# Kernel tuning notes

Measured on AMD Instinct MI355X. Metric: run time of the kernel, lower is better.

The kernel has to match this reference:

```python
import jax, jax.numpy as jnp
import numpy as np

PAA_SIZE = 64  # init_kwargs paa_size
GAF_TYPE = 'GADF'  # init_kwargs GAF_type


def setup_inputs() -> dict:
    key = jax.random.key(0)
    x = jax.random.uniform(key, (256, 4096, 32), dtype=jnp.float32)
    return {"x": x}


def reference(x):
    # x: [B, T, C]
    B, T, C = x.shape
    # --- rescale: per-sample, per-channel min-max over time axis -> [0, 1]
    x_min = jnp.min(x, axis=1, keepdims=True)
    x_max = jnp.max(x, axis=1, keepdims=True)
    r = (x - x_min) / (x_max - x_min)            # [B, T, C]
    # --- PAA: strided mean over bins of length size = T // paa_size
    size = T // PAA_SIZE
    p = r[:, : PAA_SIZE * size].reshape(B, PAA_SIZE, size, C).sum(axis=2) / size  # [B, P, C]
    # --- GAF construction
    y = jnp.sqrt(1.0 - p * p)                    # [B, P, C]
    if GAF_TYPE == 'GASF':
        # out[b,i,j,c] = x_i x_j - y_i y_j (symmetric)
        out = jnp.einsum('bic,bjc->bijc', p, p) - jnp.einsum('bic,bjc->bijc', y, y)
    else:  # 'GADF'
        # original: -transpose(y x^T - x y^T) => out[b,i,j,c] = y_i x_j - x_i y_j
        out = jnp.einsum('bic,bjc->bijc', y, p) - jnp.einsum('bic,bjc->bijc', p, y)
    return out  # [B, paa_size, paa_size, C]
```

## Files before the change

kernel.cpp:

```cpp
#include <hip/hip_runtime.h>
#include <math.h>

#define BB   256
#define TT   4096
#define CC   32
#define PP   64
#define PSTR 33

__device__ __forceinline__ float4 f4min(float4 a, float4 b) {
    return make_float4(fminf(a.x,b.x), fminf(a.y,b.y), fminf(a.z,b.z), fminf(a.w,b.w));
}
__device__ __forceinline__ float4 f4max(float4 a, float4 b) {
    return make_float4(fmaxf(a.x,b.x), fmaxf(a.y,b.y), fmaxf(a.z,b.z), fmaxf(a.w,b.w));
}
__device__ __forceinline__ void f4add(float4& a, float4 v) {
    a.x += v.x; a.y += v.y; a.z += v.z; a.w += v.w;
}
__device__ __forceinline__ float4 shflxor4(float4 v, int m) {
    return make_float4(__shfl_xor(v.x, m), __shfl_xor(v.y, m),
                       __shfl_xor(v.z, m), __shfl_xor(v.w, m));
}

__global__ __launch_bounds__(1024, 4) void gaf_kernel(const float* __restrict__ x,
                                                      float* __restrict__ out) {
    __shared__ float sp[PP * PSTR];
    __shared__ float sy[PP * PSTR];
    __shared__ float redmin[16 * CC];
    __shared__ float redmax[16 * CC];

    const int tid  = threadIdx.x;
    const int lane = tid & 63;
    const int wave = tid >> 6;
    const int cg   = lane & 7;
    const int b    = blockIdx.x;

    const float4* xw = (const float4*)x + (size_t)b * (TT * CC / 4) + wave * 2048 + lane;

    const float FBIG = 3.402823466e+38f;
    float4 mn = make_float4(FBIG, FBIG, FBIG, FBIG);
    float4 mx = make_float4(-FBIG, -FBIG, -FBIG, -FBIG);
    float4 acc[4];
    #pragma unroll
    for (int g = 0; g < 4; ++g) acc[g] = make_float4(0.f, 0.f, 0.f, 0.f);

    #pragma unroll
    for (int g = 0; g < 4; ++g) {
        float4 buf[8];
        #pragma unroll
        for (int u = 0; u < 8; ++u) buf[u] = xw[(g * 8 + u) * 64];
        #pragma unroll
        for (int u = 0; u < 8; ++u) {
            mn = f4min(mn, buf[u]); mx = f4max(mx, buf[u]); f4add(acc[g], buf[u]);
        }
    }

    #pragma unroll
    for (int m = 8; m <= 32; m <<= 1) {
        mn = f4min(mn, shflxor4(mn, m));
        mx = f4max(mx, shflxor4(mx, m));
        #pragma unroll
        for (int g = 0; g < 4; ++g) f4add(acc[g], shflxor4(acc[g], m));
    }

    if (lane < 8) {
        *(float4*)&redmin[wave * CC + cg * 4] = mn;
        *(float4*)&redmax[wave * CC + cg * 4] = mx;
    }
    __syncthreads();

    float4 gmn = *(const float4*)&redmin[0 * CC + cg * 4];
    float4 gmx = *(const float4*)&redmax[0 * CC + cg * 4];
    #pragma unroll
    for (int w = 1; w < 16; ++w) {
        gmn = f4min(gmn, *(const float4*)&redmin[w * CC + cg * 4]);
        gmx = f4max(gmx, *(const float4*)&redmax[w * CC + cg * 4]);
    }

    float4 inv;
    inv.x = 1.0f / (gmx.x - gmn.x);  inv.y = 1.0f / (gmx.y - gmn.y);
    inv.z = 1.0f / (gmx.z - gmn.z);  inv.w = 1.0f / (gmx.w - gmn.w);
    const float s64 = 1.0f / 64.0f;

    if (lane < 8) {
        #pragma unroll
        for (int g = 0; g < 4; ++g) {
            float4 p, y;
            p.x = (acc[g].x * s64 - gmn.x) * inv.x;  p.y = (acc[g].y * s64 - gmn.y) * inv.y;
            p.z = (acc[g].z * s64 - gmn.z) * inv.z;  p.w = (acc[g].w * s64 - gmn.w) * inv.w;
            y.x = sqrtf(fmaxf(1.f - p.x * p.x, 0.f));  y.y = sqrtf(fmaxf(1.f - p.y * p.y, 0.f));
            y.z = sqrtf(fmaxf(1.f - p.z * p.z, 0.f));  y.w = sqrtf(fmaxf(1.f - p.w * p.w, 0.f));
            const int s = wave * 4 + g;
            *(float4*)&sp[s * PSTR + cg * 4] = p;
            *(float4*)&sy[s * PSTR + cg * 4] = y;
        }
    }
    __syncthreads();

    const int jrow = lane >> 3;
    float4 pj[8], yj[8];
    #pragma unroll
    for (int jc = 0; jc < 8; ++jc) {
        const int j = jc * 8 + jrow;
        pj[jc] = *(const float4*)&sp[j * PSTR + cg * 4];
        yj[jc] = *(const float4*)&sy[j * PSTR + cg * 4];
    }

    float4* ob = (float4*)out + (size_t)b * (PP * PP * CC / 4) + wave * 2048 + lane;

    #pragma unroll
    for (int ii = 0; ii < 4; ++ii) {
        const int i = wave * 4 + ii;
        const float4 pi = *(const float4*)&sp[i * PSTR + cg * 4];
        const float4 yi = *(const float4*)&sy[i * PSTR + cg * 4];
        #pragma unroll
        for (int jc = 0; jc < 8; ++jc) {
            float4 r;
            r.x = yi.x * pj[jc].x - pi.x * yj[jc].x;
            r.y = yi.y * pj[jc].y - pi.y * yj[jc].y;
            r.z = yi.z * pj[jc].z - pi.z * yj[jc].z;
            r.w = yi.w * pj[jc].w - pi.w * yj[jc].w;
            ob[ii * 512 + jc * 64] = r;
        }
    }
}

extern "C" void kernel_launch(void* const* d_in, const int* in_sizes, int n_in,
                              void* d_out, int out_size, void* d_ws, size_t ws_size,
                              hipStream_t stream) {
    const float* x = (const float*)d_in[0];
    float* out = (float*)d_out;
    gaf_kernel<<<BB, 1024, 0, stream>>>(x, out);
}
```

Before: 231.3 us.

## Split fused GAF kernel into reduce and expand kernels with more blocks

Replaces the single 256-block, 1024-thread kernel with two launches. The first reduces per-chunk min/max and segment sums over 1024 blocks into workspace, and the second builds the GADF output over 2048 blocks. The aim is to occupy more compute units, since 256 blocks of 1024 threads may underfill the device and serialize the read and write phases. The cost is an extra kernel launch and a small round trip of intermediates through global memory.

Result: slower. 273.3 us (+18.2%).

```diff
diff --git a/kernel.cpp b/kernel.cpp
--- a/kernel.cpp
+++ b/kernel.cpp
@@ -21,106 +21,137 @@
                        __shfl_xor(v.z, m), __shfl_xor(v.w, m));
 }
 
-__global__ __launch_bounds__(1024, 4) void gaf_kernel(const float* __restrict__ x,
-                                                      float* __restrict__ out) {
-    __shared__ float sp[PP * PSTR];
-    __shared__ float sy[PP * PSTR];
-    __shared__ float redmin[16 * CC];
-    __shared__ float redmax[16 * CC];
+__global__ __launch_bounds__(256) void gaf_reduce(const float* __restrict__ x,
+                                                  float* __restrict__ segsum,
+                                                  float* __restrict__ pmin,
+                                                  float* __restrict__ pmax) {
+    __shared__ float redmin[4 * CC], redmax[4 * CC];
+    const int tid  = threadIdx.x;
+    const int cg   = tid & 7;
+    const int r    = tid >> 3;
+    const int wave = tid >> 6;
+    const int lane = tid & 63;
+    const int b     = blockIdx.x >> 2;
+    const int chunk = blockIdx.x & 3;
 
-    const int tid  = threadIdx.x;
-    const int lane = tid & 63;
-    const int wave = tid >> 6;
-    const int cg   = lane & 7;
-    const int b    = blockIdx.x;
-
-    const float4* xw = (const float4*)x + (size_t)b * (TT * CC / 4) + wave * 2048 + lane;
+    const float4* xp = (const float4*)x + (size_t)b * 32768 + chunk * 8192 + r * 256 + cg;
 
     const float FBIG = 3.402823466e+38f;
-    float4 mn = make_float4(FBIG, FBIG, FBIG, FBIG);
-    float4 mx = make_float4(-FBIG, -FBIG, -FBIG, -FBIG);
-    float4 acc[4];
-    #pragma unroll
-    for (int g = 0; g < 4; ++g) acc[g] = make_float4(0.f, 0.f, 0.f, 0.f);
+    float4 mn  = make_float4(FBIG, FBIG, FBIG, FBIG);
+    float4 mx  = make_float4(-FBIG, -FBIG, -FBIG, -FBIG);
+    float4 acc = make_float4(0.f, 0.f, 0.f, 0.f);
 
     #pragma unroll
     for (int g = 0; g < 4; ++g) {
         float4 buf[8];
         #pragma unroll
-        for (int u = 0; u < 8; ++u) buf[u] = xw[(g * 8 + u) * 64];
+        for (int u = 0; u < 8; ++u) buf[u] = xp[(g * 8 + u) * 8];
         #pragma unroll
         for (int u = 0; u < 8; ++u) {
-            mn = f4min(mn, buf[u]); mx = f4max(mx, buf[u]); f4add(acc[g], buf[u]);
+            mn = f4min(mn, buf[u]); mx = f4max(mx, buf[u]); f4add(acc, buf[u]);
         }
     }
+
+    float4 seg = acc;
+    f4add(seg, shflxor4(acc, 8));
 
     #pragma unroll
     for (int m = 8; m <= 32; m <<= 1) {
         mn = f4min(mn, shflxor4(mn, m));
         mx = f4max(mx, shflxor4(mx, m));
-        #pragma unroll
-        for (int g = 0; g < 4; ++g) f4add(acc[g], shflxor4(acc[g], m));
     }
-
     if (lane < 8) {
         *(float4*)&redmin[wave * CC + cg * 4] = mn;
         *(float4*)&redmax[wave * CC + cg * 4] = mx;
     }
-    __syncthreads();
 
-    float4 gmn = *(const float4*)&redmin[0 * CC + cg * 4];
-    float4 gmx = *(const float4*)&redmax[0 * CC + cg * 4];
-    #pragma unroll
-    for (int w = 1; w < 16; ++w) {
-        gmn = f4min(gmn, *(const float4*)&redmin[w * CC + cg * 4]);
-        gmx = f4max(gmx, *(const float4*)&redmax[w * CC + cg * 4]);
+    if ((r & 1) == 0) {
+        const int s = chunk * 16 + (r >> 1);
+        *(float4*)&segsum[((size_t)b * PP + s) * CC + cg * 4] = seg;
     }
 
-    float4 inv;
-    inv.x = 1.0f / (gmx.x - gmn.x);  inv.y = 1.0f / (gmx.y - gmn.y);
-    inv.z = 1.0f / (gmx.z - gmn.z);  inv.w = 1.0f / (gmx.w - gmn.w);
-    const float s64 = 1.0f / 64.0f;
+    __syncthreads();
+    if (tid < 8) {
+        float4 m0 = *(const float4*)&redmin[0 * CC + tid * 4];
+        float4 x0 = *(const float4*)&redmax[0 * CC + tid * 4];
+        #pragma unroll
+        for (int w = 1; w < 4; ++w) {
+            m0 = f4min(m0, *(const float4*)&redmin[w * CC + tid * 4]);
+            x0 = f4max(x0, *(const float4*)&redmax[w * CC + tid * 4]);
+        }
+        *(float4*)&pmin[((size_t)b * 4 + chunk) * CC + tid * 4] = m0;
+        *(float4*)&pmax[((size_t)b * 4 + chunk) * CC + tid * 4] = x0;
+    }
+}
 
-    if (lane < 8) {
+__global__ __launch_bounds__(256) void gaf_expand(const float* __restrict__ segsum,
+                                                  const float* __restrict__ pmin,
+                                                  const float* __restrict__ pmax,
+                                                  float* __restrict__ out) {
+    __shared__ float sp[PP * PSTR];
+    __shared__ float sy[PP * PSTR];
+    __shared__ float lmn[CC], linv[CC];
+
+    const int tid = threadIdx.x;
+    const int b   = blockIdx.x >> 3;
+    const int ib  = blockIdx.x & 7;
+
+    if (tid < 8) {
+        float4 mn = *(const float4*)&pmin[((size_t)b * 4 + 0) * CC + tid * 4];
+        float4 mx = *(const float4*)&pmax[((size_t)b * 4 + 0) * CC + tid * 4];
         #pragma unroll
-        for (int g = 0; g < 4; ++g) {
-            float4 p, y;
-            p.x = (acc[g].x * s64 - gmn.x) * inv.x;  p.y = (acc[g].y * s64 - gmn.y) * inv.y;
-            p.z = (acc[g].z * s64 - gmn.z) * inv.z;  p.w = (acc[g].w * s64 - gmn.w) * inv.w;
-            y.x = sqrtf(fmaxf(1.f - p.x * p.x, 0.f));  y.y = sqrtf(fmaxf(1.f - p.y * p.y, 0.f));
-            y.z = sqrtf(fmaxf(1.f - p.z * p.z, 0.f));  y.w = sqrtf(fmaxf(1.f - p.w * p.w, 0.f));
-            const int s = wave * 4 + g;
-            *(float4*)&sp[s * PSTR + cg * 4] = p;
-            *(float4*)&sy[s * PSTR + cg * 4] = y;
+        for (int c = 1; c < 4; ++c) {
+            mn = f4min(mn, *(const float4*)&pmin[((size_t)b * 4 + c) * CC + tid * 4]);
+            mx = f4max(mx, *(const float4*)&pmax[((size_t)b * 4 + c) * CC + tid * 4]);
         }
+        float4 inv;
+        inv.x = 1.0f / (mx.x - mn.x);  inv.y = 1.0f / (mx.y - mn.y);
+        inv.z = 1.0f / (mx.z - mn.z);  inv.w = 1.0f / (mx.w - mn.w);
+        *(float4*)&lmn[tid * 4]  = mn;
+        *(float4*)&linv[tid * 4] = inv;
     }
     __syncthreads();
 
-    const int jrow = lane >> 3;
-    float4 pj[8], yj[8];
+    const float s64 = 1.0f / 64.0f;
     #pragma unroll
-    for (int jc = 0; jc < 8; ++jc) {
-        const int j = jc * 8 + jrow;
-        pj[jc] = *(const float4*)&sp[j * PSTR + cg * 4];
-        yj[jc] = *(const float4*)&sy[j * PSTR + cg * 4];
+    for (int it = 0; it < 2; ++it) {
+        const int item = it * 256 + tid;
+        const int s  = item >> 3;
+        const int c  = item & 7;
+        float4 raw = *(const float4*)&segsum[((size_t)b * PP + s) * CC + c * 4];
+        float4 mn  = *(const float4*)&lmn[c * 4];
+        float4 inv = *(const float4*)&linv[c * 4];
+        float4 p, y;
+        p.x = (raw.x * s64 - mn.x) * inv.x;  p.y = (raw.y * s64 - mn.y) * inv.y;
+        p.z = (raw.z * s64 - mn.z) * inv.z;  p.w = (raw.w * s64 - mn.w) * inv.w;
+        y.x = sqrtf(fmaxf(1.f - p.x * p.x, 0.f));  y.y = sqrtf(fmaxf(1.f - p.y * p.y, 0.f));
+        y.z = sqrtf(fmaxf(1.f - p.z * p.z, 0.f));  y.w = sqrtf(fmaxf(1.f - p.w * p.w, 0.f));
+        *(float4*)&sp[s * PSTR + c * 4] = p;
+        *(float4*)&sy[s * PSTR + c * 4] = y;
     }
+    __syncthreads();
 
-    float4* ob = (float4*)out + (size_t)b * (PP * PP * CC / 4) + wave * 2048 + lane;
+    const int cg = tid & 7;
+    const int j0 = tid >> 3;
+    const float4 pj0 = *(const float4*)&sp[j0 * PSTR + cg * 4];
+    const float4 yj0 = *(const float4*)&sy[j0 * PSTR + cg * 4];
+    const float4 pj1 = *(const float4*)&sp[(j0 + 32) * PSTR + cg * 4];
+    const float4 yj1 = *(const float4*)&sy[(j0 + 32) * PSTR + cg * 4];
+
+    float4* ob = (float4*)out + (size_t)b * 32768;
 
     #pragma unroll
-    for (int ii = 0; ii < 4; ++ii) {
-        const int i = wave * 4 + ii;
+    for (int ii = 0; ii < 8; ++ii) {
+        const int i = ib * 8 + ii;
         const float4 pi = *(const float4*)&sp[i * PSTR + cg * 4];
         const float4 yi = *(const float4*)&sy[i * PSTR + cg * 4];
-        #pragma unroll
-        for (int jc = 0; jc < 8; ++jc) {
-            float4 r;
-            r.x = yi.x * pj[jc].x - pi.x * yj[jc].x;
-            r.y = yi.y * pj[jc].y - pi.y * yj[jc].y;
-            r.z = yi.z * pj[jc].z - pi.z * yj[jc].z;
-            r.w = yi.w * pj[jc].w - pi.w * yj[jc].w;
-            ob[ii * 512 + jc * 64] = r;
-        }
+        float4 r0, r1;
+        r0.x = yi.x * pj0.x - pi.x * yj0.x;  r0.y = yi.y * pj0.y - pi.y * yj0.y;
+        r0.z = yi.z * pj0.z - pi.z * yj0.z;  r0.w = yi.w * pj0.w - pi.w * yj0.w;
+        r1.x = yi.x * pj1.x - pi.x * yj1.x;  r1.y = yi.y * pj1.y - pi.y * yj1.y;
+        r1.z = yi.z * pj1.z - pi.z * yj1.z;  r1.w = yi.w * pj1.w - pi.w * yj1.w;
+        ob[i * 512 + j0 * 8 + cg]       = r0;
+        ob[i * 512 + 256 + j0 * 8 + cg] = r1;
     }
 }
 
@@ -129,5 +160,10 @@
                               hipStream_t stream) {
     const float* x = (const float*)d_in[0];
     float* out = (float*)d_out;
-    gaf_kernel<<<BB, 1024, 0, stream>>>(x, out);
+    float* segsum = (float*)d_ws;
+    float* pmin   = segsum + (size_t)BB * PP * CC;
+    float* pmax   = pmin + (size_t)BB * 4 * CC;
+
+    gaf_reduce<<<BB * 4, 256, 0, stream>>>(x, segsum, pmin, pmax);
+    gaf_expand<<<BB * 8, 256, 0, stream>>>(segsum, pmin, pmax, out);
 }
```
